# Kernel optimization log

Hardware: AMD Instinct MI355X
Metric: run time of the kernel (lower is better)

## Reference

```python
import jax, jax.numpy as jnp
import numpy as np

B, S, H, NH, T = 4, 512, 512, 8, 3
DH = H // NH
DTS = H // T  # 170, per-timescale encoder width
EPS = 1e-5

def _ln(x, g, b):
    m = jnp.mean(x, axis=-1, keepdims=True)
    v = jnp.mean((x - m) ** 2, axis=-1, keepdims=True)
    return (x - m) * jax.lax.rsqrt(v + EPS) * g + b

def _gelu(x):
    return jax.nn.gelu(x, approximate=False)

def _mha(x, qkv_W, qkv_b, out_W, out_b, mask):
    # x: [B,S,H]; qkv_W: [H,3H]; mask: [B,S,S] float additive or None
    qkv = x @ qkv_W + qkv_b
    q, k, v = jnp.split(qkv, 3, axis=-1)
    q = q.reshape(B, S, NH, DH)
    k = k.reshape(B, S, NH, DH)
    v = v.reshape(B, S, NH, DH)
    scores = jnp.einsum('bqhd,bkhd->bhqk', q, k) / jnp.sqrt(jnp.float32(DH))
    if mask is not None:
        scores = scores + mask[:, None, :, :]
    attn = jax.nn.softmax(scores, axis=-1)
    o = jnp.einsum('bhqk,bkhd->bqhd', attn, v).reshape(B, S, H)
    return o @ out_W + out_b

def setup_inputs() -> dict:
    key = jax.random.key(0)
    ks = jax.random.split(key, 32)
    r = lambda i, shape, s=0.02: (jax.random.normal(ks[i], shape, dtype=jnp.float32) * s)
    inp = {}
    inp['x'] = jax.random.normal(ks[0], (B, S, H), dtype=jnp.float32)
    inp['timestamps'] = jax.random.uniform(ks[1], (B, S), dtype=jnp.float32) * 1e6
    # per-timescale encoders (stacked over T)
    inp['enc_W'] = r(2, (T, 2, DTS), 0.5)
    inp['enc_b'] = jnp.zeros((T, DTS), jnp.float32)
    inp['enc_ln_g'] = jnp.ones((T, DTS), jnp.float32)
    inp['enc_ln_b'] = jnp.zeros((T, DTS), jnp.float32)
    # per-timescale MHA
    inp['qkv_W'] = r(3, (T, H, 3 * H))
    inp['qkv_b'] = jnp.zeros((T, 3 * H), jnp.float32)
    inp['attn_out_W'] = r(4, (T, H, H))
    inp['attn_out_b'] = jnp.zeros((T, H), jnp.float32)
    # time mixer
    inp['mixer_W1'] = r(5, (T * H, H))
    inp['mixer_b1'] = jnp.zeros((H,), jnp.float32)
    inp['mixer_ln_g'] = jnp.ones((H,), jnp.float32)
    inp['mixer_ln_b'] = jnp.zeros((H,), jnp.float32)
    inp['mixer_W2'] = r(6, (H, T))
    inp['mixer_b2'] = jnp.zeros((T,), jnp.float32)
    # transformer encoder layer (post-norm, gelu, ffn=4H)
    inp['el_qkv_W'] = r(7, (H, 3 * H))
    inp['el_qkv_b'] = jnp.zeros((3 * H,), jnp.float32)
    inp['el_out_W'] = r(8, (H, H))
    inp['el_out_b'] = jnp.zeros((H,), jnp.float32)
    inp['el_ln1_g'] = jnp.ones((H,), jnp.float32)
    inp['el_ln1_b'] = jnp.zeros((H,), jnp.float32)
    inp['el_ff_W1'] = r(9, (H, 4 * H))
    inp['el_ff_b1'] = jnp.zeros((4 * H,), jnp.float32)
    inp['el_ff_W2'] = r(10, (4 * H, H))
    inp['el_ff_b2'] = jnp.zeros((H,), jnp.float32)
    inp['el_ln2_g'] = jnp.ones((H,), jnp.float32)
    inp['el_ln2_b'] = jnp.zeros((H,), jnp.float32)
    # output projection
    inp['op_W'] = r(11, (H, H))
    inp['op_b'] = jnp.zeros((H,), jnp.float32)
    inp['op_ln_g'] = jnp.ones((H,), jnp.float32)
    inp['op_ln_b'] = jnp.zeros((H,), jnp.float32)
    return inp

def reference(x, timestamps, enc_W, enc_b, enc_ln_g, enc_ln_b, qkv_W, qkv_b, attn_out_W, attn_out_b,
              mixer_W1, mixer_b1, mixer_ln_g, mixer_ln_b, mixer_W2, mixer_b2,
              el_qkv_W, el_qkv_b, el_out_W, el_out_b, el_ln1_g, el_ln1_b,
              el_ff_W1, el_ff_b1, el_ff_W2, el_ff_b2, el_ln2_g, el_ln2_b,
              op_W, op_b, op_ln_g, op_ln_b):
    # pairwise time features [B,S,S]
    time_diff = timestamps[:, :, None] - timestamps[:, None, :]
    direction = jnp.sign(time_diff)
    magnitude = jnp.log1p(jnp.abs(time_diff) / 3600.0)
    outs = []
    for i in range(T):
        mag = magnitude / (10.0 ** i)
        tf = jnp.stack([direction, mag], axis=-1)            # [B,S,S,2]
        e = tf @ enc_W[i] + enc_b[i]                          # [B,S,S,DTS]
        e = _gelu(_ln(e, enc_ln_g[i], enc_ln_b[i]))
        mask = jnp.mean(e, axis=-1)                           # [B,S,S] additive attn mask
        outs.append(_mha(x, qkv_W[i], qkv_b[i], attn_out_W[i], attn_out_b[i], mask))
    combined = jnp.concatenate(outs, axis=-1)                 # [B,S,T*H]
    m = _gelu(_ln(combined @ mixer_W1 + mixer_b1, mixer_ln_g, mixer_ln_b))
    mix = jax.nn.softmax(m @ mixer_W2 + mixer_b2, axis=-1)    # [B,S,T]
    weighted = sum(mix[..., i:i + 1] * outs[i] for i in range(T))
    # post-norm transformer encoder layer
    sa = _mha(weighted, el_qkv_W, el_qkv_b, el_out_W, el_out_b, None)
    h1 = _ln(weighted + sa, el_ln1_g, el_ln1_b)
    ff = _gelu(h1 @ el_ff_W1 + el_ff_b1) @ el_ff_W2 + el_ff_b2
    h2 = _ln(h1 + ff, el_ln2_g, el_ln2_b)
    out = _ln(h2 @ op_W + op_b, op_ln_g, op_ln_b)
    return out
```

## Files before the change

kernel.cpp:

```cpp
#include <hip/hip_runtime.h>
#include <hip/hip_bf16.h>
#include <math.h>

#define Bq 4
#define Sq 512
#define Hq 512
#define NHq 8
#define Tq 3
#define DTSq 170
#define BSq 2048
#define NLUT 2048
#define MAGMAXf 5.6304994f

typedef float f32x4 __attribute__((ext_vector_type(4)));
typedef __bf16 bf16x4 __attribute__((ext_vector_type(4)));
typedef __bf16 bf16x8 __attribute__((ext_vector_type(8)));

__device__ __forceinline__ float gelu_f(float x){
  return 0.5f * x * (1.0f + erff(x * 0.70710678118654752f));
}

__device__ __forceinline__ void gload16(const void* g, void* l){
  __builtin_amdgcn_global_load_lds((const __attribute__((address_space(1))) void*)g,
                                   (__attribute__((address_space(3))) void*)l, 16, 0, 0);
}

__device__ __forceinline__ float waveReduceSum(float v){
  #pragma unroll
  for (int off = 32; off > 0; off >>= 1) v += __shfl_xor(v, off);
  return v;
}

__device__ __forceinline__ float blockReduce(float v, float* red){
  int tid = threadIdx.x;
  __syncthreads();
  red[tid] = v; __syncthreads();
  for (int s = 128; s > 0; s >>= 1){
    if (tid < s) red[tid] += red[tid + s];
    __syncthreads();
  }
  return red[0];
}

__global__ __launch_bounds__(256) void mask_lut_build(const float* __restrict__ encW,
                                                      const float* __restrict__ encB,
                                                      const float* __restrict__ g,
                                                      const float* __restrict__ be,
                                                      float* __restrict__ lut){
  int td = blockIdx.x;
  int t = td / 3, dsel = td % 3;
  float d = (float)(dsel - 1);
  __shared__ float red[256];
  __shared__ float sw0[DTSq], sw1[DTSq], sbc[DTSq], sg[DTSq], sbe[DTSq];
  __shared__ float sS[6];
  int tid = threadIdx.x;
  const float* W0 = encW + t * 2 * DTSq;
  const float* W1 = W0 + DTSq;
  const float* Bv = encB + t * DTSq;
  float w0 = (tid < DTSq) ? W0[tid] : 0.f;
  float w1 = (tid < DTSq) ? W1[tid] : 0.f;
  float bv = (tid < DTSq) ? Bv[tid] : 0.f;
  const float invD = 1.0f / (float)DTSq;
  float m0 = blockReduce(w0, red) * invD;
  float m1 = blockReduce(w1, red) * invD;
  float mb = blockReduce(bv, red) * invD;
  float c0 = (tid < DTSq) ? (w0 - m0) : 0.f;
  float c1 = (tid < DTSq) ? (w1 - m1) : 0.f;
  float cb = (tid < DTSq) ? (bv - mb) : 0.f;
  if (tid < DTSq){
    sw0[tid] = c0; sw1[tid] = c1; sbc[tid] = cb;
    sg[tid] = g[t * DTSq + tid]; sbe[tid] = be[t * DTSq + tid];
  }
  float pa = blockReduce(c0 * c0, red) * invD;
  float pb = blockReduce(c1 * c1, red) * invD;
  float pc = blockReduce(c0 * c1, red) * invD;
  float pd = blockReduce(c0 * cb, red) * invD;
  float pe = blockReduce(c1 * cb, red) * invD;
  float pf = blockReduce(cb * cb, red) * invD;
  if (tid == 0){ sS[0]=pa; sS[1]=pb; sS[2]=pc; sS[3]=pd; sS[4]=pe; sS[5]=pf; }
  __syncthreads();
  float A = sS[0], Bs = sS[1], Cs = sS[2], Ds = sS[3], Es = sS[4], Fs = sS[5];
  int e = blockIdx.y * 256 + tid;
  float tscale = (t == 0) ? 1.f : ((t == 1) ? 0.1f : 0.01f);
  float m = (MAGMAXf / (float)(NLUT - 1)) * (float)e * tscale;
  float var = fabsf(d) * A + m * m * Bs + Fs + 2.f * (d * m * Cs + d * Ds + m * Es);
  float rs = rsqrtf(var + 1e-5f);
  float sum = 0.f;
  for (int c = 0; c < DTSq; ++c){
    float ee = fmaf(m, sw1[c], fmaf(d, sw0[c], sbc[c]));
    float n = fmaf(ee * rs, sg[c], sbe[c]);
    sum += n * 0.5f * (1.0f + erff(n * 0.70710678118654752f));
  }
  lut[td * NLUT + e] = sum * (1.0f / (float)DTSq);
}

__global__ __launch_bounds__(256) void mask_fill(const float* __restrict__ ts,
                                                 const float* __restrict__ lut,
                                                 __bf16* __restrict__ maskbuf){
  int bi = blockIdx.x;
  int b = bi >> 9, i = bi & 511;
  float tsi = ts[bi];
  for (int j0 = 0; j0 < Sq; j0 += 256){
    int j = j0 + threadIdx.x;
    float dt = tsi - ts[(b << 9) + j];
    int dsel = (dt > 0.f) ? 2 : ((dt < 0.f) ? 0 : 1);
    float mag = log1pf(fabsf(dt) * (1.0f / 3600.0f));
    float u = mag * ((float)(NLUT - 1) / MAGMAXf);
    int i0 = (int)u; if (i0 > NLUT - 2) i0 = NLUT - 2;
    float f = u - (float)i0;
    #pragma unroll
    for (int t = 0; t < Tq; ++t){
      const float* lp = lut + (t * 3 + dsel) * NLUT + i0;
      float v = lp[0] + f * (lp[1] - lp[0]);
      maskbuf[(((size_t)(t * Bq + b) * Sq + i) * Sq) + j] = (__bf16)v;
    }
  }
}

struct CvtEnt { const float* W; __bf16* WT; int ldw, ldt, ntn, start; };
struct CvtArgs { CvtEnt e[12]; };

__global__ __launch_bounds__(256) void cvt_wT_all(CvtArgs a){
  int bid = blockIdx.x;
  int i = 0;
  #pragma unroll
  for (int k = 1; k < 12; ++k) if (bid >= a.e[k].start) i = k;
  const float* W = a.e[i].W;
  __bf16* WT = a.e[i].WT;
  int ldw = a.e[i].ldw, ldt = a.e[i].ldt;
  int local = bid - a.e[i].start;
  int tn = local % a.e[i].ntn, tk = local / a.e[i].ntn;
  int n0 = tn * 64, k0 = tk * 64;
  __shared__ float T[64][65];
  int tid = threadIdx.x;
  #pragma unroll
  for (int q = 0; q < 16; ++q){
    int lin = q * 256 + tid;
    int r = lin >> 6, c = lin & 63;
    T[r][c] = W[(size_t)(k0 + r) * ldw + n0 + c];
  }
  __syncthreads();
  #pragma unroll
  for (int q = 0; q < 16; ++q){
    int lin = q * 256 + tid;
    int n = lin >> 6, k = lin & 63;
    WT[(size_t)(n0 + n) * ldt + k0 + k] = (__bf16)T[k][n];
  }
}

__global__ __launch_bounds__(256) void cvt_bf(const float* __restrict__ in,
                                              __bf16* __restrict__ out, int n){
  int idx = (blockIdx.x * 256 + threadIdx.x) * 4;
  if (idx < n){
    float4 v = *(const float4*)&in[idx];
    bf16x4 r; r[0]=(__bf16)v.x; r[1]=(__bf16)v.y; r[2]=(__bf16)v.z; r[3]=(__bf16)v.w;
    *(bf16x4*)&out[idx] = r;
  }
}

template<int BM, int BN>
__global__ __launch_bounds__(256) void gemm_pipe(
    const __bf16* __restrict__ A, int lda, size_t sAz,
    const __bf16* __restrict__ BT, int ldb, size_t sBz,
    const float* __restrict__ bias, int sBiasz,
    float* __restrict__ C32, __bf16* __restrict__ C16, int ldc, size_t sCz,
    int K, int act)
{
  constexpr int MF = BM / 32;
  constexpr int NF = BN / 32;
  constexpr int LOADS = MF + NF;
  constexpr int ABYTES = BM * 128;
  constexpr int BBYTES = BN * 128;
  __shared__ __bf16 lds[(2 * (ABYTES + BBYTES)) / 2];
  int tid = threadIdx.x;

  int gx = gridDim.x, nwg = gx * gridDim.y;
  int lin = blockIdx.x + gx * blockIdx.y;
  int q8 = nwg >> 3;
  int swz = (lin & 7) * q8 + (lin >> 3);
  int bx = swz % gx, by = swz / gx;

  int z = blockIdx.z;
  A  += (size_t)z * sAz;
  BT += (size_t)z * sBz;
  const float* bz = bias ? bias + (size_t)z * sBiasz : nullptr;
  size_t cbase = (size_t)z * sCz;
  int brow = by * BM, bcol = bx * BN;

  int lane = tid & 63, w = tid >> 6;
  int wr = (w >> 1) * (BM / 2), wc = (w & 1) * (BN / 2);
  int lr = lane & 15, lg = lane >> 4;

  f32x4 acc[MF][NF];
  #pragma unroll
  for (int m = 0; m < MF; ++m)
    #pragma unroll
    for (int n = 0; n < NF; ++n) acc[m][n] = (f32x4){0.f, 0.f, 0.f, 0.f};

  char* lbase = (char*)lds;

  auto stage = [&](int buf, int ko){
    char* ab = lbase + buf * (ABYTES + BBYTES);
    #pragma unroll
    for (int qq = 0; qq < MF; ++qq){
      int byte = (qq * 256 + tid) * 16;
      int row = byte >> 7, col8 = byte & 127;
      int src = col8 ^ ((row & 7) << 4);
      gload16(&A[(size_t)(brow + row) * lda + ko + (src >> 1)], ab + byte);
    }
    char* bb = ab + ABYTES;
    #pragma unroll
    for (int qq = 0; qq < NF; ++qq){
      int byte = (qq * 256 + tid) * 16;
      int row = byte >> 7, col8 = byte & 127;
      int src = col8 ^ ((row & 7) << 4);
      gload16(&BT[(size_t)(bcol + row) * ldb + ko + (src >> 1)], bb + byte);
    }
  };

  stage(0, 0);
  int nk = K >> 6;
  for (int kt = 0; kt < nk; ++kt){
    int cur = kt & 1;
    if (kt + 1 < nk){
      stage(cur ^ 1, (kt + 1) << 6);
      if constexpr (LOADS == 3)      asm volatile("s_waitcnt vmcnt(3)" ::: "memory");
      else if constexpr (LOADS == 4) asm volatile("s_waitcnt vmcnt(4)" ::: "memory");
      else                           asm volatile("s_waitcnt vmcnt(6)" ::: "memory");
    } else {
      asm volatile("s_waitcnt vmcnt(0)" ::: "memory");
    }
    __builtin_amdgcn_s_barrier();
    __builtin_amdgcn_sched_barrier(0);
    char* ab = lbase + cur * (ABYTES + BBYTES);
    char* bb = ab + ABYTES;
    #pragma unroll
    for (int s = 0; s < 2; ++s){
      bf16x8 af[MF], bfr[NF];
      #pragma unroll
      for (int m = 0; m < MF; ++m){
        int row = wr + m * 16 + lr;
        int col8 = (s * 64 + lg * 16) ^ ((row & 7) << 4);
        af[m] = *(const bf16x8*)(ab + row * 128 + col8);
      }
      #pragma unroll
      for (int n = 0; n < NF; ++n){
        int row = wc + n * 16 + lr;
        int col8 = (s * 64 + lg * 16) ^ ((row & 7) << 4);
        bfr[n] = *(const bf16x8*)(bb + row * 128 + col8);
      }
      #pragma unroll
      for (int m = 0; m < MF; ++m)
        #pragma unroll
        for (int n = 0; n < NF; ++n)
          acc[m][n] = __builtin_amdgcn_mfma_f32_16x16x32_bf16(af[m], bfr[n], acc[m][n], 0, 0, 0);
    }
    asm volatile("" ::: "memory");
    __builtin_amdgcn_s_barrier();
  }

  #pragma unroll
  for (int m = 0; m < MF; ++m){
    #pragma unroll
    for (int n = 0; n < NF; ++n){
      int col = bcol + wc + n * 16 + lr;
      float bv = bz ? bz[col] : 0.f;
      #pragma unroll
      for (int j = 0; j < 4; ++j){
        int row = brow + wr + m * 16 + lg * 4 + j;
        float v = acc[m][n][j] + bv;
        if (act) v = gelu_f(v);
        size_t idx = cbase + (size_t)row * ldc + col;
        if (C32) C32[idx] = v;
        if (C16) C16[idx] = (__bf16)v;
      }
    }
  }
}

template<bool HM>
__global__ __launch_bounds__(256) void flash_attn(
    const __bf16* __restrict__ qkv, size_t sQz,
    const __bf16* __restrict__ vt,  size_t sVz,
    const __bf16* __restrict__ mask, size_t sMz,
    __bf16* __restrict__ ctx, size_t sCz)
{
  int t = blockIdx.z;
  qkv += (size_t)t * sQz;
  vt  += (size_t)t * sVz;
  ctx += (size_t)t * sCz;
  const __bf16* mk = HM ? mask + (size_t)t * sMz : nullptr;

  int lin = blockIdx.x + (blockIdx.y << 3);
  int swz = (lin & 7) * 32 + (lin >> 3);
  int io = (swz & 7) * 64;
  int bh = swz >> 3;
  int b = bh >> 3, h = bh & 7;

  constexpr int TB = 8192;
  constexpr int BUFB = HM ? 3 * TB : 2 * TB;
  __shared__ char lds[2 * BUFB + (HM ? 0 : TB)];
  char* lb = lds;
  int tid = threadIdx.x, lane = tid & 63, w = tid >> 6;
  int lr = lane & 15, lg = lane >> 4;

  const __bf16* qrow = &qkv[(size_t)(b * Sq + io + w * 16 + lr) * 1536 + h * 64];
  bf16x8 q0 = *(const bf16x8*)&qrow[lg * 8];
  bf16x8 q1 = *(const bf16x8*)&qrow[32 + lg * 8];

  auto stage = [&](int buf, int jo){
    char* kb = lb + buf * BUFB;
    #pragma unroll
    for (int qq = 0; qq < 2; ++qq){
      int byte = (qq * 256 + tid) * 16;
      int row = byte >> 7;
      int src = (byte & 127) ^ ((row & 7) << 4);
      gload16(&qkv[(size_t)(b * Sq + jo + row) * 1536 + 512 + h * 64 + (src >> 1)], kb + byte);
    }
    char* vb = kb + TB;
    #pragma unroll
    for (int qq = 0; qq < 2; ++qq){
      int byte = (qq * 256 + tid) * 16;
      int row = byte >> 7;
      int src = (byte & 127) ^ ((row & 7) << 4);
      gload16(&vt[((size_t)bh * 64 + row) * Sq + jo + (src >> 1)], vb + byte);
    }
    if constexpr (HM){
      char* mb = vb + TB;
      #pragma unroll
      for (int qq = 0; qq < 2; ++qq){
        int byte = (qq * 256 + tid) * 16;
        int row = byte >> 7;
        int src = (byte & 127) ^ ((row & 7) << 4);
        gload16(&mk[(size_t)(b * Sq + io + row) * Sq + jo + (src >> 1)], mb + byte);
      }
    }
  };

  f32x4 o[4];
  #pragma unroll
  for (int n = 0; n < 4; ++n) o[n] = (f32x4){0.f, 0.f, 0.f, 0.f};
  float mrow[4] = {-1e30f, -1e30f, -1e30f, -1e30f};
  float lrow[4] = {0.f, 0.f, 0.f, 0.f};

  stage(0, 0);
  #pragma unroll
  for (int kt = 0; kt < 8; ++kt){
    int cur = kt & 1;

    if (kt + 1 < 8){
      stage(cur ^ 1, (kt + 1) << 6);
      if constexpr (HM) asm volatile("s_waitcnt vmcnt(6)" ::: "memory");
      else              asm volatile("s_waitcnt vmcnt(4)" ::: "memory");
    } else {
      asm volatile("s_waitcnt vmcnt(0)" ::: "memory");
    }
    __builtin_amdgcn_s_barrier();
    __builtin_amdgcn_sched_barrier(0);

    char* kb = lb + cur * BUFB;
    char* vb = kb + TB;
    char* mb = HM ? vb + TB : lb + 2 * BUFB;

    f32x4 s4[4];
    #pragma unroll
    for (int n = 0; n < 4; ++n) s4[n] = (f32x4){0.f, 0.f, 0.f, 0.f};
    __builtin_amdgcn_s_setprio(1);
    #pragma unroll
    for (int s = 0; s < 2; ++s){
      bf16x8 aq = s ? q1 : q0;
      #pragma unroll
      for (int n = 0; n < 4; ++n){
        int row = n * 16 + lr;
        int colb = (s * 64 + lg * 16) ^ ((row & 7) << 4);
        bf16x8 bk = *(const bf16x8*)(kb + row * 128 + colb);
        s4[n] = __builtin_amdgcn_mfma_f32_16x16x32_bf16(aq, bk, s4[n], 0, 0, 0);
      }
    }
    __builtin_amdgcn_s_setprio(0);

    float sv[4][4];
    #pragma unroll
    for (int n = 0; n < 4; ++n){
      #pragma unroll
      for (int reg = 0; reg < 4; ++reg){
        float v = s4[n][reg] * 0.125f;
        if constexpr (HM){
          int row = w * 16 + lg * 4 + reg;
          int off = ((n * 16 + lr) * 2) ^ ((row & 7) << 4);
          v += (float)*(const __bf16*)(mb + row * 128 + off);
        }
        sv[n][reg] = v;
      }
    }

    #pragma unroll
    for (int reg = 0; reg < 4; ++reg){
      float pmax = fmaxf(fmaxf(sv[0][reg], sv[1][reg]), fmaxf(sv[2][reg], sv[3][reg]));
      #pragma unroll
      for (int off = 1; off < 16; off <<= 1) pmax = fmaxf(pmax, __shfl_xor(pmax, off));
      if (pmax > mrow[reg] + 8.0f){
        float corr = __expf(mrow[reg] - pmax);
        mrow[reg] = pmax;
        lrow[reg] *= corr;
        #pragma unroll
        for (int n = 0; n < 4; ++n) o[n][reg] *= corr;
      }
      float rs = 0.f;
      #pragma unroll
      for (int n = 0; n < 4; ++n){
        float p = __expf(sv[n][reg] - mrow[reg]);
        sv[n][reg] = p;
        rs += p;
      }
      #pragma unroll
      for (int off = 1; off < 16; off <<= 1) rs += __shfl_xor(rs, off);
      lrow[reg] += rs;
    }

    #pragma unroll
    for (int n = 0; n < 4; ++n)
      #pragma unroll
      for (int reg = 0; reg < 4; ++reg){
        int row = w * 16 + lg * 4 + reg;
        int off = ((n * 16 + lr) * 2) ^ ((row & 7) << 4);
        *(__bf16*)(mb + row * 128 + off) = (__bf16)sv[n][reg];
      }
    __builtin_amdgcn_s_setprio(1);
    #pragma unroll
    for (int s = 0; s < 2; ++s){
      int arow = w * 16 + lr;
      int acol = (s * 64 + lg * 16) ^ ((arow & 7) << 4);
      bf16x8 ap = *(const bf16x8*)(mb + arow * 128 + acol);
      #pragma unroll
      for (int n = 0; n < 4; ++n){
        int row = n * 16 + lr;
        int colb = (s * 64 + lg * 16) ^ ((row & 7) << 4);
        bf16x8 bv = *(const bf16x8*)(vb + row * 128 + colb);
        o[n] = __builtin_amdgcn_mfma_f32_16x16x32_bf16(ap, bv, o[n], 0, 0, 0);
      }
    }
    __builtin_amdgcn_s_setprio(0);

    asm volatile("" ::: "memory");
    __builtin_amdgcn_s_barrier();
  }

  #pragma unroll
  for (int reg = 0; reg < 4; ++reg){
    float inv = 1.0f / lrow[reg];
    int row = b * Sq + io + w * 16 + lg * 4 + reg;
    #pragma unroll
    for (int n = 0; n < 4; ++n)
      ctx[(size_t)row * Hq + h * 64 + n * 16 + lr] = (__bf16)(o[n][reg] * inv);
  }
}

__global__ __launch_bounds__(256) void ln_rows(const float* __restrict__ in,
                                               const float* __restrict__ res,
                                               const float* __restrict__ g,
                                               const float* __restrict__ bb,
                                               float* __restrict__ out32,
                                               __bf16* __restrict__ out16,
                                               int do_gelu){
  int row = blockIdx.x * 4 + (threadIdx.x >> 6);
  int lane = threadIdx.x & 63;
  const float* ir = in + (size_t)row * Hq;
  const float* rr = res ? res + (size_t)row * Hq : nullptr;
  float x[8]; float s = 0.f, sq = 0.f;
  #pragma unroll
  for (int k = 0; k < 8; ++k){
    int c = lane + 64 * k;
    float v = ir[c];
    if (rr) v += rr[c];
    x[k] = v; s += v; sq += v * v;
  }
  s = waveReduceSum(s); sq = waveReduceSum(sq);
  float mean = s * (1.0f / Hq);
  float var = fmaxf(sq * (1.0f / Hq) - mean * mean, 0.f);
  float rstd = rsqrtf(var + 1e-5f);
  #pragma unroll
  for (int k = 0; k < 8; ++k){
    int c = lane + 64 * k;
    float y = (x[k] - mean) * rstd * g[c] + bb[c];
    if (do_gelu) y = gelu_f(y);
    if (out32) out32[(size_t)row * Hq + c] = y;
    if (out16) out16[(size_t)row * Hq + c] = (__bf16)y;
  }
}

__global__ __launch_bounds__(256) void ln_mixer_weighted(const float* __restrict__ in,
                                                         const float* __restrict__ g,
                                                         const float* __restrict__ bb,
                                                         const float* __restrict__ W2,
                                                         const float* __restrict__ b2,
                                                         const __bf16* __restrict__ comb,
                                                         float* __restrict__ out32,
                                                         __bf16* __restrict__ out16){
  int row = blockIdx.x * 4 + (threadIdx.x >> 6);
  int lane = threadIdx.x & 63;
  const float* ir = in + (size_t)row * Hq;
  float x[8]; float s = 0.f, sq = 0.f;
  #pragma unroll
  for (int k = 0; k < 8; ++k){
    int c = lane + 64 * k;
    float v = ir[c];
    x[k] = v; s += v; sq += v * v;
  }
  s = waveReduceSum(s); sq = waveReduceSum(sq);
  float mean = s * (1.0f / Hq);
  float var = fmaxf(sq * (1.0f / Hq) - mean * mean, 0.f);
  float rstd = rsqrtf(var + 1e-5f);
  float a0 = 0.f, a1 = 0.f, a2 = 0.f;
  #pragma unroll
  for (int k = 0; k < 8; ++k){
    int c = lane + 64 * k;
    float y = gelu_f((x[k] - mean) * rstd * g[c] + bb[c]);
    const float* wv = W2 + c * 3;
    a0 = fmaf(y, wv[0], a0); a1 = fmaf(y, wv[1], a1); a2 = fmaf(y, wv[2], a2);
  }
  a0 = waveReduceSum(a0) + b2[0];
  a1 = waveReduceSum(a1) + b2[1];
  a2 = waveReduceSum(a2) + b2[2];
  float mx = fmaxf(a0, fmaxf(a1, a2));
  float e0 = __expf(a0 - mx), e1 = __expf(a1 - mx), e2 = __expf(a2 - mx);
  float inv = 1.0f / (e0 + e1 + e2);
  float m0 = e0 * inv, m1 = e1 * inv, m2 = e2 * inv;
  const __bf16* cr = comb + (size_t)row * 1536;
  #pragma unroll
  for (int k = 0; k < 8; ++k){
    int c = lane + 64 * k;
    float v = m0 * (float)cr[c] + m1 * (float)cr[512 + c] + m2 * (float)cr[1024 + c];
    out32[(size_t)row * Hq + c] = v;
    out16[(size_t)row * Hq + c] = (__bf16)v;
  }
}

__global__ __launch_bounds__(256) void transpose_v(const __bf16* __restrict__ qkv, size_t sQz,
                                                   __bf16* __restrict__ vt, size_t sVz){
  int t = blockIdx.z;
  qkv += (size_t)t * sQz;
  vt  += (size_t)t * sVz;
  int bh = blockIdx.y, b = bh >> 3, h = bh & 7;
  int so = blockIdx.x * 64;
  __shared__ __bf16 T[64][72];
  int tid = threadIdx.x;
  #pragma unroll
  for (int q = 0; q < 16; ++q){
    int lin = q * 256 + tid;
    int r = lin >> 6, c = lin & 63;
    T[r][c] = qkv[(size_t)(b * Sq + so + r) * 1536 + 1024 + h * 64 + c];
  }
  __syncthreads();
  #pragma unroll
  for (int q = 0; q < 16; ++q){
    int lin = q * 256 + tid;
    int d = lin >> 6, s = lin & 63;
    vt[((size_t)bh * 64 + d) * Sq + so + s] = T[s][d];
  }
}

extern "C" void kernel_launch(void* const* d_in, const int* in_sizes, int n_in,
                              void* d_out, int out_size, void* d_ws, size_t ws_size,
                              hipStream_t stream){
  const float* x         = (const float*)d_in[0];
  const float* ts        = (const float*)d_in[1];
  const float* enc_W     = (const float*)d_in[2];
  const float* enc_b     = (const float*)d_in[3];
  const float* enc_ln_g  = (const float*)d_in[4];
  const float* enc_ln_b  = (const float*)d_in[5];
  const float* qkv_W     = (const float*)d_in[6];
  const float* qkv_b     = (const float*)d_in[7];
  const float* aout_W    = (const float*)d_in[8];
  const float* aout_b    = (const float*)d_in[9];
  const float* mx_W1     = (const float*)d_in[10];
  const float* mx_b1     = (const float*)d_in[11];
  const float* mx_ln_g   = (const float*)d_in[12];
  const float* mx_ln_b   = (const float*)d_in[13];
  const float* mx_W2     = (const float*)d_in[14];
  const float* mx_b2     = (const float*)d_in[15];
  const float* el_qkv_W  = (const float*)d_in[16];
  const float* el_qkv_b  = (const float*)d_in[17];
  const float* el_out_W  = (const float*)d_in[18];
  const float* el_out_b  = (const float*)d_in[19];
  const float* el_ln1_g  = (const float*)d_in[20];
  const float* el_ln1_b  = (const float*)d_in[21];
  const float* el_ff_W1  = (const float*)d_in[22];
  const float* el_ff_b1  = (const float*)d_in[23];
  const float* el_ff_W2  = (const float*)d_in[24];
  const float* el_ff_b2  = (const float*)d_in[25];
  const float* el_ln2_g  = (const float*)d_in[26];
  const float* el_ln2_b  = (const float*)d_in[27];
  const float* op_W      = (const float*)d_in[28];
  const float* op_b      = (const float*)d_in[29];
  const float* op_ln_g   = (const float*)d_in[30];
  const float* op_ln_b   = (const float*)d_in[31];

  float* ws = (float*)d_ws;
  size_t o = 0;
  __bf16* MASKBb = (__bf16*)(ws + o); o += 1572864;
  __bf16* XB     = (__bf16*)(ws + o); o += 524288;
  __bf16* qkvT   = (__bf16*)(ws + o); o += 1179648;
  __bf16* aoutT  = (__bf16*)(ws + o); o += 393216;
  __bf16* mx1T   = (__bf16*)(ws + o); o += 393216;
  __bf16* elqkvT = (__bf16*)(ws + o); o += 393216;
  __bf16* eloutT = (__bf16*)(ws + o); o += 131072;
  __bf16* ff1T   = (__bf16*)(ws + o); o += 524288;
  __bf16* ff2T   = (__bf16*)(ws + o); o += 524288;
  __bf16* opT    = (__bf16*)(ws + o); o += 131072;
  __bf16* QKVb   = (__bf16*)(ws + o); o += 4718592;
  __bf16* VTb    = (__bf16*)(ws + o); o += 1572864;
  __bf16* FFBb   = (__bf16*)(ws + o); o += 2097152;
  __bf16* CTXb   = (__bf16*)(ws + o); o += 1572864;
  __bf16* COMBb  = (__bf16*)(ws + o); o += 1572864;
  float*  MBUF   = ws + o;            o += 1048576;
  float*  WEI    = ws + o;            o += 1048576;
  __bf16* WEIb   = (__bf16*)(ws + o); o += 524288;
  float*  SA     = ws + o;            o += 1048576;
  float*  H1     = ws + o;            o += 1048576;
  __bf16* H1b    = (__bf16*)(ws + o); o += 524288;
  float*  H2     = ws + o;            o += 1048576;
  __bf16* H2b    = (__bf16*)(ws + o); o += 524288;
  float*  LUTB   = ws + o;            o += 9 * NLUT;
  float*  OPO    = MBUF;

  cvt_bf<<<1024, 256, 0, stream>>>(x, XB, BSq * Hq);
  {
    CvtArgs ca;
    for (int t = 0; t < 3; ++t)
      ca.e[t] = {qkv_W + (size_t)t * 512 * 1536, qkvT + (size_t)t * 1536 * 512, 1536, 512, 24, 192 * t};
    for (int t = 0; t < 3; ++t)
      ca.e[3 + t] = {aout_W + (size_t)t * 512 * 512, aoutT + (size_t)t * 512 * 512, 512, 512, 8, 576 + 64 * t};
    ca.e[6]  = {mx_W1,    mx1T,   512,  1536, 8,  768};
    ca.e[7]  = {el_qkv_W, elqkvT, 1536, 512,  24, 960};
    ca.e[8]  = {el_out_W, eloutT, 512,  512,  8,  1152};
    ca.e[9]  = {el_ff_W1, ff1T,   2048, 512,  32, 1216};
    ca.e[10] = {el_ff_W2, ff2T,   512,  2048, 8,  1472};
    ca.e[11] = {op_W,     opT,    512,  512,  8,  1728};
    cvt_wT_all<<<1792, 256, 0, stream>>>(ca);
  }

  mask_lut_build<<<dim3(9, NLUT / 256), 256, 0, stream>>>(enc_W, enc_b, enc_ln_g, enc_ln_b, LUTB);
  mask_fill<<<BSq, 256, 0, stream>>>(ts, LUTB, MASKBb);

  gemm_pipe<128,64><<<dim3(24, 16, 3), 256, 0, stream>>>(XB, 512, 0, qkvT, 512, (size_t)1536 * 512,
      qkv_b, 1536, nullptr, QKVb, 1536, (size_t)2048 * 1536, 512, 0);
  transpose_v<<<dim3(8, 32, 3), 256, 0, stream>>>(QKVb, (size_t)2048 * 1536, VTb, (size_t)32 * 64 * 512);
  flash_attn<true><<<dim3(8, 32, 3), 256, 0, stream>>>(QKVb, (size_t)2048 * 1536,
      VTb, (size_t)32 * 64 * 512, MASKBb, (size_t)4 * 512 * 512, CTXb, (size_t)2048 * 512);
  gemm_pipe<64,32><<<dim3(16, 32, 3), 256, 0, stream>>>(CTXb, 512, (size_t)2048 * 512, aoutT, 512, (size_t)512 * 512,
      aout_b, 512, nullptr, COMBb, 1536, 512, 512, 0);

  gemm_pipe<64,32><<<dim3(16, 32, 1), 256, 0, stream>>>(COMBb, 1536, 0, mx1T, 1536, 0,
      mx_b1, 0, MBUF, nullptr, 512, 0, 1536, 0);
  ln_mixer_weighted<<<512, 256, 0, stream>>>(MBUF, mx_ln_g, mx_ln_b, mx_W2, mx_b2, COMBb, WEI, WEIb);

  gemm_pipe<128,64><<<dim3(24, 16, 1), 256, 0, stream>>>(WEIb, 512, 0, elqkvT, 512, 0,
      el_qkv_b, 0, nullptr, QKVb, 1536, 0, 512, 0);
  transpose_v<<<dim3(8, 32, 1), 256, 0, stream>>>(QKVb, 0, VTb, 0);
  flash_attn<false><<<dim3(8, 32, 1), 256, 0, stream>>>(QKVb, 0, VTb, 0, nullptr, 0, CTXb, 0);
  gemm_pipe<64,32><<<dim3(16, 32, 1), 256, 0, stream>>>(CTXb, 512, 0, eloutT, 512, 0,
      el_out_b, 0, SA, nullptr, 512, 0, 512, 0);
  ln_rows<<<512, 256, 0, stream>>>(WEI, SA, el_ln1_g, el_ln1_b, H1, H1b, 0);
  gemm_pipe<128,64><<<dim3(32, 16, 1), 256, 0, stream>>>(H1b, 512, 0, ff1T, 512, 0,
      el_ff_b1, 0, nullptr, FFBb, 2048, 0, 512, 1);
  gemm_pipe<64,32><<<dim3(16, 32, 1), 256, 0, stream>>>(FFBb, 2048, 0, ff2T, 2048, 0,
      el_ff_b2, 0, SA, nullptr, 512, 0, 2048, 0);
  ln_rows<<<512, 256, 0, stream>>>(H1, SA, el_ln2_g, el_ln2_b, H2, H2b, 0);

  gemm_pipe<64,32><<<dim3(16, 32, 1), 256, 0, stream>>>(H2b, 512, 0, opT, 512, 0,
      op_b, 0, OPO, nullptr, 512, 0, 512, 0);
  ln_rows<<<512, 256, 0, stream>>>(OPO, nullptr, op_ln_g, op_ln_b, (float*)d_out, nullptr, 0);
}
```

Baseline: 214.9 us.

## Merge prep kernels, fuse V transpose into QKV GEMM epilogue, restructure pipeline waits

```diff
diff --git a/kernel.cpp b/kernel.cpp
--- a/kernel.cpp
+++ b/kernel.cpp
@@ -42,18 +42,59 @@
   return red[0];
 }
 
-__global__ __launch_bounds__(256) void mask_lut_build(const float* __restrict__ encW,
-                                                      const float* __restrict__ encB,
-                                                      const float* __restrict__ g,
-                                                      const float* __restrict__ be,
-                                                      float* __restrict__ lut){
-  int td = blockIdx.x;
-  int t = td / 3, dsel = td % 3;
-  float d = (float)(dsel - 1);
+struct CvtEnt { const float* W; __bf16* WT; int ldw, ldt, ntn, start; };
+struct CvtArgs { CvtEnt e[12]; };
+
+__global__ __launch_bounds__(256) void prep_all(
+    const float* __restrict__ x, __bf16* __restrict__ xb,
+    CvtArgs a,
+    const float* __restrict__ encW, const float* __restrict__ encB,
+    const float* __restrict__ g, const float* __restrict__ be,
+    float* __restrict__ lut)
+{
+  __shared__ float T[64][65];
   __shared__ float red[256];
   __shared__ float sw0[DTSq], sw1[DTSq], sbc[DTSq], sg[DTSq], sbe[DTSq];
   __shared__ float sS[6];
-  int tid = threadIdx.x;
+  int bid = blockIdx.x, tid = threadIdx.x;
+
+  if (bid < 1024){
+    int idx = (bid * 256 + tid) * 4;
+    float4 v = *(const float4*)&x[idx];
+    bf16x4 r; r[0]=(__bf16)v.x; r[1]=(__bf16)v.y; r[2]=(__bf16)v.z; r[3]=(__bf16)v.w;
+    *(bf16x4*)&xb[idx] = r;
+    return;
+  }
+  if (bid < 1024 + 1792){
+    int wb = bid - 1024;
+    int i = 0;
+    #pragma unroll
+    for (int k = 1; k < 12; ++k) if (wb >= a.e[k].start) i = k;
+    const float* W = a.e[i].W;
+    __bf16* WT = a.e[i].WT;
+    int ldw = a.e[i].ldw, ldt = a.e[i].ldt;
+    int local = wb - a.e[i].start;
+    int tn = local % a.e[i].ntn, tk = local / a.e[i].ntn;
+    int n0 = tn * 64, k0 = tk * 64;
+    #pragma unroll
+    for (int q = 0; q < 16; ++q){
+      int lin = q * 256 + tid;
+      int r = lin >> 6, c = lin & 63;
+      T[r][c] = W[(size_t)(k0 + r) * ldw + n0 + c];
+    }
+    __syncthreads();
+    #pragma unroll
+    for (int q = 0; q < 16; ++q){
+      int lin = q * 256 + tid;
+      int n = lin >> 6, k = lin & 63;
+      WT[(size_t)(n0 + n) * ldt + k0 + k] = (__bf16)T[k][n];
+    }
+    return;
+  }
+  int local = bid - (1024 + 1792);
+  int td = local >> 3, echunk = local & 7;
+  int t = td / 3, dsel = td % 3;
+  float d = (float)(dsel - 1);
   const float* W0 = encW + t * 2 * DTSq;
   const float* W1 = W0 + DTSq;
   const float* Bv = encB + t * DTSq;
@@ -80,7 +121,7 @@
   if (tid == 0){ sS[0]=pa; sS[1]=pb; sS[2]=pc; sS[3]=pd; sS[4]=pe; sS[5]=pf; }
   __syncthreads();
   float A = sS[0], Bs = sS[1], Cs = sS[2], Ds = sS[3], Es = sS[4], Fs = sS[5];
-  int e = blockIdx.y * 256 + tid;
+  int e = echunk * 256 + tid;
   float tscale = (t == 0) ? 1.f : ((t == 1) ? 0.1f : 0.01f);
   float m = (MAGMAXf / (float)(NLUT - 1)) * (float)e * tscale;
   float var = fabsf(d) * A + m * m * Bs + Fs + 2.f * (d * m * Cs + d * Ds + m * Es);
@@ -117,58 +158,17 @@
   }
 }
 
-struct CvtEnt { const float* W; __bf16* WT; int ldw, ldt, ntn, start; };
-struct CvtArgs { CvtEnt e[12]; };
-
-__global__ __launch_bounds__(256) void cvt_wT_all(CvtArgs a){
-  int bid = blockIdx.x;
-  int i = 0;
-  #pragma unroll
-  for (int k = 1; k < 12; ++k) if (bid >= a.e[k].start) i = k;
-  const float* W = a.e[i].W;
-  __bf16* WT = a.e[i].WT;
-  int ldw = a.e[i].ldw, ldt = a.e[i].ldt;
-  int local = bid - a.e[i].start;
-  int tn = local % a.e[i].ntn, tk = local / a.e[i].ntn;
-  int n0 = tn * 64, k0 = tk * 64;
-  __shared__ float T[64][65];
-  int tid = threadIdx.x;
-  #pragma unroll
-  for (int q = 0; q < 16; ++q){
-    int lin = q * 256 + tid;
-    int r = lin >> 6, c = lin & 63;
-    T[r][c] = W[(size_t)(k0 + r) * ldw + n0 + c];
-  }
-  __syncthreads();
-  #pragma unroll
-  for (int q = 0; q < 16; ++q){
-    int lin = q * 256 + tid;
-    int n = lin >> 6, k = lin & 63;
-    WT[(size_t)(n0 + n) * ldt + k0 + k] = (__bf16)T[k][n];
-  }
-}
-
-__global__ __launch_bounds__(256) void cvt_bf(const float* __restrict__ in,
-                                              __bf16* __restrict__ out, int n){
-  int idx = (blockIdx.x * 256 + threadIdx.x) * 4;
-  if (idx < n){
-    float4 v = *(const float4*)&in[idx];
-    bf16x4 r; r[0]=(__bf16)v.x; r[1]=(__bf16)v.y; r[2]=(__bf16)v.z; r[3]=(__bf16)v.w;
-    *(bf16x4*)&out[idx] = r;
-  }
-}
-
 template<int BM, int BN>
 __global__ __launch_bounds__(256) void gemm_pipe(
     const __bf16* __restrict__ A, int lda, size_t sAz,
     const __bf16* __restrict__ BT, int ldb, size_t sBz,
     const float* __restrict__ bias, int sBiasz,
     float* __restrict__ C32, __bf16* __restrict__ C16, int ldc, size_t sCz,
+    __bf16* __restrict__ VT, size_t sVTz,
     int K, int act)
 {
   constexpr int MF = BM / 32;
   constexpr int NF = BN / 32;
-  constexpr int LOADS = MF + NF;
   constexpr int ABYTES = BM * 128;
   constexpr int BBYTES = BN * 128;
   __shared__ __bf16 lds[(2 * (ABYTES + BBYTES)) / 2];
@@ -222,16 +222,10 @@
   int nk = K >> 6;
   for (int kt = 0; kt < nk; ++kt){
     int cur = kt & 1;
-    if (kt + 1 < nk){
-      stage(cur ^ 1, (kt + 1) << 6);
-      if constexpr (LOADS == 3)      asm volatile("s_waitcnt vmcnt(3)" ::: "memory");
-      else if constexpr (LOADS == 4) asm volatile("s_waitcnt vmcnt(4)" ::: "memory");
-      else                           asm volatile("s_waitcnt vmcnt(6)" ::: "memory");
-    } else {
-      asm volatile("s_waitcnt vmcnt(0)" ::: "memory");
-    }
+    asm volatile("s_waitcnt vmcnt(0)" ::: "memory");
     __builtin_amdgcn_s_barrier();
     __builtin_amdgcn_sched_barrier(0);
+    if (kt + 1 < nk) stage(cur ^ 1, (kt + 1) << 6);
     char* ab = lbase + cur * (ABYTES + BBYTES);
     char* bb = ab + ABYTES;
     #pragma unroll
@@ -255,10 +249,9 @@
         for (int n = 0; n < NF; ++n)
           acc[m][n] = __builtin_amdgcn_mfma_f32_16x16x32_bf16(af[m], bfr[n], acc[m][n], 0, 0, 0);
     }
-    asm volatile("" ::: "memory");
-    __builtin_amdgcn_s_barrier();
-  }
-
+  }
+
+  bool doVT = (VT != nullptr) && (bcol + wc >= 1024);
   #pragma unroll
   for (int m = 0; m < MF; ++m){
     #pragma unroll
@@ -273,6 +266,12 @@
         size_t idx = cbase + (size_t)row * ldc + col;
         if (C32) C32[idx] = v;
         if (C16) C16[idx] = (__bf16)v;
+        if (doVT){
+          int hc = col - 1024;
+          VT[(size_t)z * sVTz +
+             (((size_t)((row >> 9) * 8 + (hc >> 6)) * 64 + (hc & 63)) << 9) + (row & 511)]
+            = (__bf16)v;
+        }
       }
     }
   }
@@ -347,16 +346,10 @@
   #pragma unroll
   for (int kt = 0; kt < 8; ++kt){
     int cur = kt & 1;
-
-    if (kt + 1 < 8){
-      stage(cur ^ 1, (kt + 1) << 6);
-      if constexpr (HM) asm volatile("s_waitcnt vmcnt(6)" ::: "memory");
-      else              asm volatile("s_waitcnt vmcnt(4)" ::: "memory");
-    } else {
-      asm volatile("s_waitcnt vmcnt(0)" ::: "memory");
-    }
+    asm volatile("s_waitcnt vmcnt(0)" ::: "memory");
     __builtin_amdgcn_s_barrier();
     __builtin_amdgcn_sched_barrier(0);
+    if (kt + 1 < 8) stage(cur ^ 1, (kt + 1) << 6);
 
     char* kb = lb + cur * BUFB;
     char* vb = kb + TB;
@@ -441,9 +434,6 @@
       }
     }
     __builtin_amdgcn_s_setprio(0);
-
-    asm volatile("" ::: "memory");
-    __builtin_amdgcn_s_barrier();
   }
 
   #pragma unroll
@@ -533,30 +523,6 @@
     float v = m0 * (float)cr[c] + m1 * (float)cr[512 + c] + m2 * (float)cr[1024 + c];
     out32[(size_t)row * Hq + c] = v;
     out16[(size_t)row * Hq + c] = (__bf16)v;
-  }
-}
-
-__global__ __launch_bounds__(256) void transpose_v(const __bf16* __restrict__ qkv, size_t sQz,
-                                                   __bf16* __restrict__ vt, size_t sVz){
-  int t = blockIdx.z;
-  qkv += (size_t)t * sQz;
-  vt  += (size_t)t * sVz;
-  int bh = blockIdx.y, b = bh >> 3, h = bh & 7;
-  int so = blockIdx.x * 64;
-  __shared__ __bf16 T[64][72];
-  int tid = threadIdx.x;
-  #pragma unroll
-  for (int q = 0; q < 16; ++q){
-    int lin = q * 256 + tid;
-    int r = lin >> 6, c = lin & 63;
-    T[r][c] = qkv[(size_t)(b * Sq + so + r) * 1536 + 1024 + h * 64 + c];
-  }
-  __syncthreads();
-  #pragma unroll
-  for (int q = 0; q < 16; ++q){
-    int lin = q * 256 + tid;
-    int d = lin >> 6, s = lin & 63;
-    vt[((size_t)bh * 64 + d) * Sq + so + s] = T[s][d];
   }
 }
 
@@ -624,7 +590,6 @@
   float*  LUTB   = ws + o;            o += 9 * NLUT;
   float*  OPO    = MBUF;
 
-  cvt_bf<<<1024, 256, 0, stream>>>(x, XB, BSq * Hq);
   {
     CvtArgs ca;
     for (int t = 0; t < 3; ++t)
@@ -637,38 +602,35 @@
     ca.e[9]  = {el_ff_W1, ff1T,   2048, 512,  32, 1216};
     ca.e[10] = {el_ff_W2, ff2T,   512,  2048, 8,  1472};
     ca.e[11] = {op_W,     opT,    512,  512,  8,  1728};
-    cvt_wT_all<<<1792, 256, 0, stream>>>(ca);
-  }
-
-  mask_lut_build<<<dim3(9, NLUT / 256), 256, 0, stream>>>(enc_W, enc_b, enc_ln_g, enc_ln_b, LUTB);
+    prep_all<<<1024 + 1792 + 72, 256, 0, stream>>>(x, XB, ca, enc_W, enc_b,
+                                                   enc_ln_g, enc_ln_b, LUTB);
+  }
   mask_fill<<<BSq, 256, 0, stream>>>(ts, LUTB, MASKBb);
 
   gemm_pipe<128,64><<<dim3(24, 16, 3), 256, 0, stream>>>(XB, 512, 0, qkvT, 512, (size_t)1536 * 512,
-      qkv_b, 1536, nullptr, QKVb, 1536, (size_t)2048 * 1536, 512, 0);
-  transpose_v<<<dim3(8, 32, 3), 256, 0, stream>>>(QKVb, (size_t)2048 * 1536, VTb, (size_t)32 * 64 * 512);
+      qkv_b, 1536, nullptr, QKVb, 1536, (size_t)2048 * 1536, VTb, (size_t)32 * 64 * 512, 512, 0);
   flash_attn<true><<<dim3(8, 32, 3), 256, 0, stream>>>(QKVb, (size_t)2048 * 1536,
       VTb, (size_t)32 * 64 * 512, MASKBb, (size_t)4 * 512 * 512, CTXb, (size_t)2048 * 512);
   gemm_pipe<64,32><<<dim3(16, 32, 3), 256, 0, stream>>>(CTXb, 512, (size_t)2048 * 512, aoutT, 512, (size_t)512 * 512,
-      aout_b, 512, nullptr, COMBb, 1536, 512, 512, 0);
+      aout_b, 512, nullptr, COMBb, 1536, 512, nullptr, 0, 512, 0);
 
   gemm_pipe<64,32><<<dim3(16, 32, 1), 256, 0, stream>>>(COMBb, 1536, 0, mx1T, 1536, 0,
-      mx_b1, 0, MBUF, nullptr, 512, 0, 1536, 0);
+      mx_b1, 0, MBUF, nullptr, 512, 0, nullptr, 0, 1536, 0);
   ln_mixer_weighted<<<512, 256, 0, stream>>>(MBUF, mx_ln_g, mx_ln_b, mx_W2, mx_b2, COMBb, WEI, WEIb);
 
   gemm_pipe<128,64><<<dim3(24, 16, 1), 256, 0, stream>>>(WEIb, 512, 0, elqkvT, 512, 0,
-      el_qkv_b, 0, nullptr, QKVb, 1536, 0, 512, 0);
-  transpose_v<<<dim3(8, 32, 1), 256, 0, stream>>>(QKVb, 0, VTb, 0);
+      el_qkv_b, 0, nullptr, QKVb, 1536, 0, VTb, 0, 512, 0);
   flash_attn<false><<<dim3(8, 32, 1), 256, 0, stream>>>(QKVb, 0, VTb, 0, nullptr, 0, CTXb, 0);
   gemm_pipe<64,32><<<dim3(16, 32, 1), 256, 0, stream>>>(CTXb, 512, 0, eloutT, 512, 0,
-      el_out_b, 0, SA, nullptr, 512, 0, 512, 0);
+      el_out_b, 0, SA, nullptr, 512, 0, nullptr, 0, 512, 0);
   ln_rows<<<512, 256, 0, stream>>>(WEI, SA, el_ln1_g, el_ln1_b, H1, H1b, 0);
   gemm_pipe<128,64><<<dim3(32, 16, 1), 256, 0, stream>>>(H1b, 512, 0, ff1T, 512, 0,
-      el_ff_b1, 0, nullptr, FFBb, 2048, 0, 512, 1);
+      el_ff_b1, 0, nullptr, FFBb, 2048, 0, nullptr, 0, 512, 1);
   gemm_pipe<64,32><<<dim3(16, 32, 1), 256, 0, stream>>>(FFBb, 2048, 0, ff2T, 2048, 0,
-      el_ff_b2, 0, SA, nullptr, 512, 0, 2048, 0);
+      el_ff_b2, 0, SA, nullptr, 512, 0, nullptr, 0, 2048, 0);
   ln_rows<<<512, 256, 0, stream>>>(H1, SA, el_ln2_g, el_ln2_b, H2, H2b, 0);
 
   gemm_pipe<64,32><<<dim3(16, 32, 1), 256, 0, stream>>>(H2b, 512, 0, opT, 512, 0,
-      op_b, 0, OPO, nullptr, 512, 0, 512, 0);
+      op_b, 0, OPO, nullptr, 512, 0, nullptr, 0, 512, 0);
   ln_rows<<<512, 256, 0, stream>>>(OPO, nullptr, op_ln_g, op_ln_b, (float*)d_out, nullptr, 0);
 }
```

Measured after the change: 224.5 us. 4.5% more time.
